# Optimization experiments

Measured on AMD Instinct MI355X. Metric: run time of the kernel, lower is better.

The kernel has to match this reference:

```python
import jax, jax.numpy as jnp
import numpy as np

NUM_V = 20000
N_EDGES = 160000
IN_CH, OUT_CH = 16, 32
IN_ORDER = OUT_ORDER = MID_ORDER = 2
N_RINGS = 2
BAND_LIMIT = 2
NUM_SAMPLES = 7


def build_kernel_basis(n_in, n_out, bl):
    """Equivariant kernel basis [num_bases, 2*bl+1, 2*n_out+1, 2*n_in+1].
    Freq axis layout: [const, cos(t), sin(t), cos(2t), sin(2t), ...] matching precomp."""
    Din, Dout, F = 2 * n_in + 1, 2 * n_out + 1, 2 * bl + 1
    I = np.eye(2)
    E = np.array([[0., -1.], [1., 0.]])   # rotation by pi/2
    S = np.array([[1., 0.], [0., -1.]])   # reflection
    ES = E @ S
    sl = lambda m: slice(0, 1) if m == 0 else slice(2 * m - 1, 2 * m + 1)
    bases = []

    def add(f, cos_blk, sin_blk, m, n):
        if f > bl:
            return
        B = np.zeros((F, Dout, Din))
        if f == 0:
            B[0, sl(m), sl(n)] = cos_blk
        else:
            B[2 * f - 1, sl(m), sl(n)] = cos_blk
            B[2 * f, sl(m), sl(n)] = sin_blk
        bases.append(B)

    for m in range(n_out + 1):
        for n in range(n_in + 1):
            if m == 0 and n == 0:
                add(0, np.ones((1, 1)), None, 0, 0)
            elif n == 0:  # scalar -> order-m pair: R(m t) e1, R(m t) e2
                add(m, np.array([[1.], [0.]]), np.array([[0.], [1.]]), m, 0)
                add(m, np.array([[0.], [1.]]), np.array([[-1.], [0.]]), m, 0)
            elif m == 0:  # order-n pair -> scalar: rows of R(-n t)
                add(n, np.array([[1., 0.]]), np.array([[0., 1.]]), 0, n)
                add(n, np.array([[0., 1.]]), np.array([[-1., 0.]]), 0, n)
            else:
                d = m - n
                f = abs(d)
                sg = 1.0 if d >= 0 else -1.0
                add(f, I, sg * E, m, n)          # R(d t)
                add(f, E, -sg * I, m, n)         # R(d t + pi/2)
                add(m + n, S, ES, m, n)          # R((m+n) t) S
                add(m + n, ES, -S, m, n)         # R((m+n) t + pi/2) S
    return np.stack(bases).astype(np.float32)


def fourier_mats(order, n):
    th = 2 * np.pi * np.arange(n) / n
    cols = [np.ones(n)]
    for m in range(1, order + 1):
        cols += [np.cos(m * th), np.sin(m * th)]
    T = np.stack(cols, 1)                              # [n_samples, 2*order+1]
    scale = np.array([1.0] + [2.0] * (2 * order)) / n
    Tinv = (T * scale).T                               # [2*order+1, n_samples]
    return jnp.asarray(T, jnp.float32), jnp.asarray(Tinv, jnp.float32)


def rep_act(x, alpha, order):
    """Gauge transport: rotate order-m feature pairs by m*alpha. x: [E,C,2*order+1]."""
    parts = [x[:, :, :1]]
    for m in range(1, order + 1):
        c = jnp.cos(m * alpha)[:, None]
        s = jnp.sin(m * alpha)[:, None]
        a, b = x[:, :, 2 * m - 1], x[:, :, 2 * m]
        parts.append(jnp.stack([c * a - s * b, s * a + c * b], axis=-1))
    return jnp.concatenate(parts, axis=-1)


def gem_conv(x, edge_index, precomp, connection, K, W, b, in_order):
    src, dst = edge_index[1], edge_index[0]
    xt = rep_act(x[src], connection, in_order)               # [E, Cin, Din] gather + transport
    wk = jnp.einsum('bfij,broc->froicj', K, W)               # fold basis with ring weights (small)
    t = jnp.einsum('ecj,froicj->efroi', xt, wk)              # per-edge freq/ring responses
    msg = jnp.einsum('efr,efroi->eoi', precomp, t)           # [E, Cout, Dout]
    out = jax.ops.segment_sum(msg, dst, num_segments=NUM_V)  # scatter-add to vertices
    return out.at[:, :, 0].add(b)                            # bias on scalar component


def regular_relu(x, order):
    T, Tinv = fourier_mats(order, NUM_SAMPLES)
    s = jnp.einsum('vcd,sd->vcs', x, T)   # irrep -> regular samples
    return jnp.einsum('vcs,ds->vcd', jax.nn.relu(s), Tinv)


def setup_inputs() -> dict:
    key = jax.random.key(0)
    k = jax.random.split(key, 8)
    nb = build_kernel_basis(IN_ORDER, MID_ORDER, BAND_LIMIT).shape[0]  # 19
    Din = 2 * IN_ORDER + 1
    x = jax.random.normal(k[0], (NUM_V, IN_CH, Din), jnp.float32)
    edge_index = jax.random.randint(k[1], (2, N_EDGES), 0, NUM_V, dtype=jnp.int32)
    precomp = jax.random.normal(k[2], (N_EDGES, 2 * BAND_LIMIT + 1, N_RINGS), jnp.float32)
    connection = jax.random.uniform(k[3], (N_EDGES,), jnp.float32) * (2 * np.pi)
    W1 = jax.random.normal(k[4], (nb, N_RINGS, OUT_CH, IN_CH), jnp.float32) * 0.1
    W2 = jax.random.normal(k[5], (nb, N_RINGS, OUT_CH, OUT_CH), jnp.float32) * 0.05
    W_lin = jax.random.normal(k[6], (OUT_CH, IN_CH), jnp.float32) * 0.1
    zeros = lambda: jnp.zeros((OUT_CH,), jnp.float32)
    return {"x": x, "edge_index": edge_index, "precomp": precomp, "connection": connection,
            "W1": W1, "b1": zeros(), "W2": W2, "b2": zeros(), "W_lin": W_lin, "b_lin": zeros()}


def reference(x, edge_index, precomp, connection, W1, b1, W2, b2, W_lin, b_lin):
    K = jnp.asarray(build_kernel_basis(IN_ORDER, MID_ORDER, BAND_LIMIT))  # orders equal -> shared basis
    y = gem_conv(x, edge_index, precomp, connection, K, W1, b1, IN_ORDER)
    y = regular_relu(y, MID_ORDER)
    y = gem_conv(y, edge_index, precomp, connection, K, W2, b2, MID_ORDER)
    res = jnp.einsum('vcd,oc->vod', x, W_lin) + b_lin[None, :, None]  # 1x1 conv residual
    o = min(y.shape[2], res.shape[2])
    y = y.at[:, :, :o].add(res[:, :, :o])
    return regular_relu(y, OUT_ORDER)
```

## Files before the change

kernel.cpp:

```cpp
#include <hip/hip_runtime.h>
#include <hip/hip_bf16.h>
#include <cstdint>

#define NV     20000
#define NE     160000
#define IC1    16
#define OC     32
#define DIN    5
#define NSLOT  49
#define NOUT   160
struct SlotTables {
    int n;
    int b[64], f[64], i[64], j[64];
    float v[64];
};

constexpr SlotTables make_slots() {
    SlotTables T{};
    float K[19][5][5][5] = {};
    int nb = 0;
    const int BL = 2;
    auto add = [&](int f, const float (*cb)[2], const float (*sb)[2],
                   int m, int n) {
        if (f > BL) return;
        int r0 = (m == 0) ? 0 : (2 * m - 1), nr = (m == 0) ? 1 : 2;
        int c0 = (n == 0) ? 0 : (2 * n - 1), nc = (n == 0) ? 1 : 2;
        for (int a = 0; a < nr; a++)
            for (int bb = 0; bb < nc; bb++) {
                if (f == 0) {
                    K[nb][0][r0 + a][c0 + bb] = cb[a][bb];
                } else {
                    K[nb][2 * f - 1][r0 + a][c0 + bb] = cb[a][bb];
                    K[nb][2 * f    ][r0 + a][c0 + bb] = sb[a][bb];
                }
            }
        nb++;
    };
    const float ONE[2][2]  = {{1, 0}, {0, 0}};
    const float I2[2][2]   = {{1, 0}, {0, 1}};
    const float E2[2][2]   = {{0, -1}, {1, 0}};
    const float S2[2][2]   = {{1, 0}, {0, -1}};
    const float ES2[2][2]  = {{0, 1}, {1, 0}};
    const float NS2[2][2]  = {{-1, 0}, {0, 1}};
    const float C10[2][2]  = {{1, 0}, {0, 0}};
    const float C01[2][2]  = {{0, 0}, {1, 0}};
    const float CM10[2][2] = {{-1, 0}, {0, 0}};
    const float R10[2][2]  = {{1, 0}, {0, 0}};
    const float R01[2][2]  = {{0, 1}, {0, 0}};
    const float RM10[2][2] = {{-1, 0}, {0, 0}};

    for (int m = 0; m <= 2; m++)
        for (int n = 0; n <= 2; n++) {
            if (m == 0 && n == 0) {
                add(0, ONE, ONE, 0, 0);
            } else if (n == 0) {
                add(m, C10, C01, m, 0);
                add(m, C01, CM10, m, 0);
            } else if (m == 0) {
                add(n, R10, R01, 0, n);
                add(n, R01, RM10, 0, n);
            } else {
                int d = m - n;
                int f = d >= 0 ? d : -d;
                float sg = d >= 0 ? 1.f : -1.f;
                const float sgE[2][2]  = {{0, -sg}, {sg, 0}};
                const float msgI[2][2] = {{-sg, 0}, {0, -sg}};
                add(f, I2, sgE, m, n);
                add(f, E2, msgI, m, n);
                add(m + n, S2, ES2, m, n);
                add(m + n, ES2, NS2, m, n);
            }
        }
    T.n = 0;
    for (int i = 0; i < 5; i++)
        for (int b = 0; b < nb; b++)
            for (int f = 0; f < 5; f++)
                for (int j = 0; j < 5; j++)
                    if (K[b][f][i][j] != 0.0f) {
                        T.b[T.n] = b; T.f[T.n] = f; T.i[T.n] = i;
                        T.j[T.n] = j; T.v[T.n] = K[b][f][i][j];
                        T.n++;
                    }
    return T;
}

constexpr SlotTables SL = make_slots();
static_assert(SL.n == NSLOT, "expect 49 kernel-basis nonzeros");

__device__ __forceinline__ uint32_t bf16_rne(float f) {
    uint32_t u = __float_as_uint(f);
    u += 0x7fffu + ((u >> 16) & 1u);
    return u >> 16;
}

typedef __attribute__((ext_vector_type(8))) short bf16x8;
typedef __attribute__((ext_vector_type(4))) float f32x4;

template<int C>
__global__ __launch_bounds__(256) void build_M(const float* __restrict__ W,
                                               float* __restrict__ M) {
    int t = blockIdx.x * 256 + threadIdx.x;
    const int K = C * 50;
    if (t >= K * NOUT) return;
    int n = t % NOUT, k = t / NOUT;
    int o = n / 5, i = n % 5;
    int c = k / 50, r50 = k % 50;
    int j = r50 / 10, q = r50 % 10;
    int f = q >> 1, r = q & 1;
    float acc = 0.f;
    #pragma unroll
    for (int s = 0; s < NSLOT; s++) {
        if (SL.j[s] == j && SL.f[s] == f && SL.i[s] == i)
            acc += SL.v[s] * W[(size_t)((SL.b[s] * 2 + r) * 32 + o) * C + c];
    }
    M[(size_t)k * NOUT + n] = acc;
}

template<int K>
__global__ __launch_bounds__(256) void build_Mfrag(const float* __restrict__ M,
                                                   uint32_t* __restrict__ Mf) {
    int t = blockIdx.x * 256 + threadIdx.x;
    const int total = (K / 32) * 10 * 64 * 4;
    if (t >= total) return;
    int a = t & 3;
    int idx = t >> 2;
    int lane = idx & 63; idx >>= 6;
    int nt = idx % 10;
    int ck = idx / 10;
    int col = nt * 16 + (lane & 15);
    int k0 = ck * 32 + (lane >> 4) * 8 + 2 * a;
    uint32_t lo = bf16_rne(M[(size_t)k0 * NOUT + col]);
    uint32_t hi = bf16_rne(M[(size_t)(k0 + 1) * NOUT + col]);
    Mf[t] = lo | (hi << 16);
}

__global__ __launch_bounds__(256) void hist_k(const int* __restrict__ ei,
                                              int* __restrict__ counts) {
    int e = blockIdx.x * 256 + threadIdx.x;
    if (e < NE) atomicAdd(&counts[ei[e]], 1);
}

__global__ __launch_bounds__(1024) void scan_k(const int* __restrict__ counts,
                                               int* __restrict__ cursor) {
    __shared__ int part[1024];
    int t = threadIdx.x;
    int base = t * 20;
    int local[20];
    int s = 0;
    #pragma unroll
    for (int k = 0; k < 20; k++) {
        int idx = base + k;
        int c = (idx < NV) ? counts[idx] : 0;
        local[k] = c; s += c;
    }
    part[t] = s;
    __syncthreads();
    for (int off = 1; off < 1024; off <<= 1) {
        int add = (t >= off) ? part[t - off] : 0;
        __syncthreads();
        part[t] += add;
        __syncthreads();
    }
    int run = (t == 0) ? 0 : part[t - 1];
    #pragma unroll
    for (int k = 0; k < 20; k++) {
        int idx = base + k;
        if (idx < NV) { cursor[idx] = run; run += local[k]; }
    }
}

__global__ __launch_bounds__(256) void scatter_pack(const int* __restrict__ ei,
                                                    const float* __restrict__ pre,
                                                    const float* __restrict__ conn,
                                                    int* __restrict__ cursor,
                                                    int* __restrict__ SRC,
                                                    float4* __restrict__ REC) {
    int e = blockIdx.x * 256 + threadIdx.x;
    if (e == 0) {
        SRC[NE] = 0;
        REC[(size_t)NE * 3 + 0] = float4{0.f, 0.f, 0.f, 0.f};
        REC[(size_t)NE * 3 + 1] = float4{0.f, 0.f, 0.f, 0.f};
        REC[(size_t)NE * 3 + 2] = float4{0.f, 0.f, 0.f, 0.f};
    }
    if (e >= NE) return;
    int pos = atomicAdd(&cursor[ei[e]], 1);
    SRC[pos] = ei[NE + e];
    float al = conn[e];
    float c1 = __cosf(al), s1 = __sinf(al);
    const float* pp = pre + (size_t)e * 10;
    REC[(size_t)pos * 3 + 0] = float4{c1, s1, pp[0], pp[1]};
    REC[(size_t)pos * 3 + 1] = float4{pp[2], pp[3], pp[4], pp[5]};
    REC[(size_t)pos * 3 + 2] = float4{pp[6], pp[7], pp[8], pp[9]};
}

__global__ __launch_bounds__(256) void x_pack(const float* __restrict__ x,
                                              uint4* __restrict__ xb) {
    int t = blockIdx.x * 256 + threadIdx.x;
    if (t >= NV * IC1) return;
    const float* xr = x + (size_t)t * 5;
    uint4 o;
    o.x = bf16_rne(xr[0]) | (bf16_rne(xr[1]) << 16);
    o.y = bf16_rne(xr[2]) | (bf16_rne(xr[3]) << 16);
    o.z = bf16_rne(xr[4]);
    o.w = 0;
    xb[t] = o;
}

template<int C>
__global__ __launch_bounds__(256) void zbuild6(const uint4* __restrict__ xb,
                                               const int*   __restrict__ SRC,
                                               const float4* __restrict__ REC,
                                               const int* __restrict__ cursor,
                                               uint32_t* __restrict__ Z,
                                               int v0, int v1) {
    __shared__ uint32_t st[3200];
    int tid = threadIdx.x;
    int t = blockIdx.x * 256 + tid;
    int pair = t >> 1, h = t & 1;
    int npairs = (v1 - v0) * C;
    bool valid = pair < npairs;
    int c = pair % C;
    int v = v0 + (valid ? pair / C : 0);
    int beg = 0, end = 0;
    if (valid) { beg = (v == 0) ? 0 : cursor[v - 1]; end = cursor[v]; }

    float acc[25];
    #pragma unroll
    for (int z = 0; z < 25; z++) acc[z] = 0.f;

    int k = beg;
    if (k < end) {
        int k1 = (k + 1 < end) ? k + 1 : NE;
        int k2 = (k + 2 < end) ? k + 2 : NE;
        int s0 = SRC[k], s1i = SRC[k1], s2i = SRC[k2];
        const float4* rp = REC + (size_t)k * 3;
        float4 r0 = rp[0], r1 = rp[1], r2 = rp[2];
        uint4 u0 = xb[(size_t)s0 * C + c];
        uint4 u1 = xb[(size_t)s1i * C + c];
        while (true) {
            bool more = (k1 != NE);
            int k3 = (k + 3 < end) ? k + 3 : NE;
            int s3i = SRC[k3];
            uint4 u2 = xb[(size_t)s2i * C + c];
            const float4* rpn = REC + (size_t)k1 * 3;
            float4 n0 = rpn[0], n1 = rpn[1], n2 = rpn[2];
            float x0 = __uint_as_float(u0.x << 16);
            float x1 = __uint_as_float(u0.x & 0xffff0000u);
            float x2 = __uint_as_float(u0.y << 16);
            float x3 = __uint_as_float(u0.y & 0xffff0000u);
            float x4 = __uint_as_float(u0.z << 16);
            float cc1 = r0.x, ss1 = r0.y;
            float cc2 = cc1 * cc1 - ss1 * ss1, ss2 = 2.f * cc1 * ss1;
            float xt[5];
            xt[0] = x0;
            xt[1] = cc1 * x1 - ss1 * x2;
            xt[2] = ss1 * x1 + cc1 * x2;
            xt[3] = cc2 * x3 - ss2 * x4;
            xt[4] = ss2 * x3 + cc2 * x4;
            float ph[5];
            ph[0] = h ? r1.w : r0.z;
            ph[1] = h ? r2.x : r0.w;
            ph[2] = h ? r2.y : r1.x;
            ph[3] = h ? r2.z : r1.y;
            ph[4] = h ? r2.w : r1.z;
            #pragma unroll
            for (int j = 0; j < 5; j++)
                #pragma unroll
                for (int w = 0; w < 5; w++)
                    acc[j * 5 + w] = fmaf(xt[j], ph[w], acc[j * 5 + w]);
            if (!more) break;
            k = k1; k1 = k2; k2 = k3;
            r0 = n0; r1 = n1; r2 = n2;
            u0 = u1; u1 = u2;
            s2i = s3i;
        }
    }
    uint32_t* sb = st + (tid >> 1) * 25;
    #pragma unroll
    for (int j = 0; j < 5; j++) {
        float q5v = __shfl_xor(acc[j * 5 + 0], 1);
        if (h == 0) {
            sb[j * 5 + 0] = bf16_rne(acc[j * 5 + 0]) | (bf16_rne(acc[j * 5 + 1]) << 16);
            sb[j * 5 + 1] = bf16_rne(acc[j * 5 + 2]) | (bf16_rne(acc[j * 5 + 3]) << 16);
            sb[j * 5 + 2] = bf16_rne(acc[j * 5 + 4]) | (bf16_rne(q5v) << 16);
        } else {
            sb[j * 5 + 3] = bf16_rne(acc[j * 5 + 1]) | (bf16_rne(acc[j * 5 + 2]) << 16);
            sb[j * 5 + 4] = bf16_rne(acc[j * 5 + 3]) | (bf16_rne(acc[j * 5 + 4]) << 16);
        }
    }
    __syncthreads();
    size_t gbase = (size_t)blockIdx.x * 3200;
    int pbase = blockIdx.x * 128;
    for (int i = tid; i < 3200; i += 256)
        if (pbase + i / 25 < npairs) Z[gbase + i] = st[i];
}

template<int K>
__global__ __launch_bounds__(256) void gemm_mfma(const uint32_t* __restrict__ Z,
                                                 const uint32_t* __restrict__ Mf,
                                                 float* __restrict__ Y,
                                                 int rows) {
    constexpr int NC = K / 32;
    __shared__ uint4 Bs[2][640];
    int t = threadIdx.x;
    int lane = t & 63;
    int wave = t >> 6;
    int r0 = blockIdx.x * 64 + wave * 16;
    int mrow = lane & 15;
    int q = lane >> 4;
    int ra = r0 + mrow;
    if (ra >= rows) ra = rows - 1;
    const uint32_t* za = Z + (size_t)ra * (K / 2) + q * 4;
    const uint4* mfg = (const uint4*)Mf + lane;

    auto stage = [&](int ck, int nb) {
        const uint4* gp = mfg + (size_t)ck * 640;
        for (int i = wave; i < 10; i += 4)
            __builtin_amdgcn_global_load_lds(
                (const __attribute__((address_space(1))) void*)(gp + i * 64),
                (__attribute__((address_space(3))) void*)(&Bs[nb][i * 64]),
                16, 0, 0);
    };

    f32x4 acc[10];
    #pragma unroll
    for (int nt = 0; nt < 10; nt++) acc[nt] = {0.f, 0.f, 0.f, 0.f};

    stage(0, 0);
    bf16x8 af = *(const bf16x8*)za;
    __syncthreads();

    for (int ck = 0; ck < NC; ck++) {
        int buf = ck & 1;
        bf16x8 af_n = af;
        if (ck + 1 < NC) {
            stage(ck + 1, buf ^ 1);
            af_n = *(const bf16x8*)(za + (ck + 1) * 16);
        }
        bf16x8 bf[10];
        #pragma unroll
        for (int nt = 0; nt < 10; nt++)
            bf[nt] = *(const bf16x8*)&Bs[buf][nt * 64 + lane];
        #pragma unroll
        for (int nt = 0; nt < 10; nt++)
            acc[nt] = __builtin_amdgcn_mfma_f32_16x16x32_bf16(af, bf[nt],
                                                              acc[nt], 0, 0, 0);
        af = af_n;
        __syncthreads();
    }
    #pragma unroll
    for (int reg = 0; reg < 4; reg++) {
        int rr = r0 + q * 4 + reg;
        if (rr < rows) {
            float* yb = Y + (size_t)rr * NOUT + (lane & 15);
            #pragma unroll
            for (int nt = 0; nt < 10; nt++) yb[nt * 16] = acc[nt][reg];
        }
    }
}

__device__ __forceinline__ void fourier_relu(float d0, float d1, float d2,
                                             float d3, float d4, float* out5) {
    float o0 = 0, o1 = 0, o2 = 0, o3 = 0, o4 = 0;
    #pragma unroll
    for (int k = 0; k < 7; k++) {
        float th = (float)k * (6.28318530717958647692f / 7.0f);
        float ck = __cosf(th), sk = __sinf(th);
        float c2k = ck * ck - sk * sk, s2k = 2.f * ck * sk;
        float sv = d0 + ck * d1 + sk * d2 + c2k * d3 + s2k * d4;
        sv = fmaxf(sv, 0.f);
        o0 += sv; o1 += sv * ck; o2 += sv * sk; o3 += sv * c2k; o4 += sv * s2k;
    }
    const float i7 = 1.0f / 7.0f;
    out5[0] = o0 * i7; out5[1] = o1 * (2.f * i7); out5[2] = o2 * (2.f * i7);
    out5[3] = o3 * (2.f * i7); out5[4] = o4 * (2.f * i7);
}

__global__ __launch_bounds__(256) void relu_mid(const float* __restrict__ y,
                                                const float* __restrict__ b1,
                                                uint4* __restrict__ yb) {
    int t = blockIdx.x * 256 + threadIdx.x;
    if (t >= NV * 32) return;
    int ch = t & 31;
    const float* yr = y + (size_t)t * 5;
    float r[5];
    fourier_relu(yr[0] + b1[ch], yr[1], yr[2], yr[3], yr[4], r);
    uint4 o;
    o.x = bf16_rne(r[0]) | (bf16_rne(r[1]) << 16);
    o.y = bf16_rne(r[2]) | (bf16_rne(r[3]) << 16);
    o.z = bf16_rne(r[4]);
    o.w = 0;
    yb[t] = o;
}

__global__ __launch_bounds__(256) void final_k(const float* __restrict__ y2,
                                               const float* __restrict__ x,
                                               const float* __restrict__ Wl,
                                               const float* __restrict__ bl,
                                               const float* __restrict__ b2,
                                               float* __restrict__ out) {
    int t = blockIdx.x * 256 + threadIdx.x;
    if (t >= NV * 32) return;
    int o = t & 31;
    int v = t >> 5;
    float r0 = 0, r1 = 0, r2 = 0, r3 = 0, r4 = 0;
    const float* xb = x + (size_t)v * (IC1 * DIN);
    const float* wl = Wl + o * IC1;
    #pragma unroll
    for (int c = 0; c < IC1; c++) {
        float w = wl[c];
        r0 = fmaf(w, xb[c*5+0], r0); r1 = fmaf(w, xb[c*5+1], r1);
        r2 = fmaf(w, xb[c*5+2], r2); r3 = fmaf(w, xb[c*5+3], r3);
        r4 = fmaf(w, xb[c*5+4], r4);
    }
    float blo = bl[o];
    const float* yb = y2 + (size_t)t * 5;
    float d0 = yb[0] + b2[o] + r0 + blo;
    float d1 = yb[1] + r1 + blo;
    float d2 = yb[2] + r2 + blo;
    float d3 = yb[3] + r3 + blo;
    float d4 = yb[4] + r4 + blo;
    float r[5];
    fourier_relu(d0, d1, d2, d3, d4, r);
    float* ob = out + (size_t)t * 5;
    #pragma unroll
    for (int d = 0; d < 5; d++) ob[d] = r[d];
}

extern "C" void kernel_launch(void* const* d_in, const int* in_sizes, int n_in,
                              void* d_out, int out_size, void* d_ws, size_t ws_size,
                              hipStream_t stream) {
    const float* x    = (const float*)d_in[0];
    const int*   ei   = (const int*)  d_in[1];
    const float* pre  = (const float*)d_in[2];
    const float* conn = (const float*)d_in[3];
    const float* W1   = (const float*)d_in[4];
    const float* b1   = (const float*)d_in[5];
    const float* W2   = (const float*)d_in[6];
    const float* b2   = (const float*)d_in[7];
    const float* Wl   = (const float*)d_in[8];
    const float* bl   = (const float*)d_in[9];
    float* out = (float*)d_out;

    const int K1 = IC1 * 50;
    const int K2 = OC  * 50;

    const size_t Y_BYTES   = (size_t)NV * NOUT * sizeof(float);
    const size_t M1_BYTES  = (size_t)K1 * NOUT * sizeof(float);
    const size_t M2_BYTES  = (size_t)K2 * NOUT * sizeof(float);
    const size_t MF1_BYTES = (size_t)(K1 / 32) * 10 * 64 * 16;
    const size_t MF2_BYTES = (size_t)(K2 / 32) * 10 * 64 * 16;
    const size_t CSR_BYTES = (size_t)(2 * NV) * sizeof(int);
    const size_t REC_BYTES = (size_t)(NE + 1) * 48;
    const size_t SRC_BYTES = (((size_t)(NE + 1) * 4 + 15) / 16) * 16;
    const size_t Y1B_BYTES = (size_t)NV * OC * 16;
    char* ws = (char*)d_ws;
    float* y1 = (float*)(ws);
    float* y2 = y1;
    float* M1 = (float*)(ws + Y_BYTES);
    float* M2 = (float*)(ws + Y_BYTES + M1_BYTES);
    uint32_t* Mf1 = (uint32_t*)(ws + Y_BYTES + M1_BYTES + M2_BYTES);
    uint32_t* Mf2 = (uint32_t*)(ws + Y_BYTES + M1_BYTES + M2_BYTES + MF1_BYTES);
    int* counts = (int*)(ws + Y_BYTES + M1_BYTES + M2_BYTES + MF1_BYTES + MF2_BYTES);
    int* cursor = counts + NV;
    size_t csr_end = Y_BYTES + M1_BYTES + M2_BYTES + MF1_BYTES + MF2_BYTES
                   + CSR_BYTES;
    float4* REC = (float4*)(ws + csr_end);
    int*    SRC = (int*)(ws + csr_end + REC_BYTES);
    uint4*  Y1B = (uint4*)(ws + csr_end + REC_BYTES + SRC_BYTES);
    uint4*  XB1 = Y1B;
    size_t fixed = csr_end + REC_BYTES + SRC_BYTES + Y1B_BYTES;

    size_t tail = (ws_size > fixed) ? (ws_size - fixed) : 0;
    uint32_t* zbuf;
    size_t zcap;
    if (tail >= Y_BYTES) { zbuf = (uint32_t*)(ws + fixed); zcap = tail; }
    else                 { zbuf = (uint32_t*)d_out;        zcap = Y_BYTES; }
    int chunk1 = (int)(zcap / ((size_t)K1 * 2)); if (chunk1 > NV) chunk1 = NV;
    int chunk2 = (int)(zcap / ((size_t)K2 * 2)); if (chunk2 > NV) chunk2 = NV;

    hipMemsetAsync(counts, 0, NV * sizeof(int), stream);

    build_M<IC1><<<(K1 * NOUT + 255) / 256, 256, 0, stream>>>(W1, M1);
    build_M<OC> <<<(K2 * NOUT + 255) / 256, 256, 0, stream>>>(W2, M2);
    build_Mfrag<K1><<<((K1 / 32) * 2560 + 255) / 256, 256, 0, stream>>>(M1, Mf1);
    build_Mfrag<K2><<<((K2 / 32) * 2560 + 255) / 256, 256, 0, stream>>>(M2, Mf2);

    hist_k<<<(NE + 255) / 256, 256, 0, stream>>>(ei, counts);
    scan_k<<<1, 1024, 0, stream>>>(counts, cursor);
    scatter_pack<<<(NE + 255) / 256, 256, 0, stream>>>(ei, pre, conn, cursor,
                                                       SRC, REC);
    x_pack<<<(NV * IC1 + 255) / 256, 256, 0, stream>>>(x, XB1);

    for (int v0 = 0; v0 < NV; v0 += chunk1) {
        int v1 = v0 + chunk1; if (v1 > NV) v1 = NV;
        int rows = v1 - v0;
        zbuild6<IC1><<<((size_t)rows * IC1 * 2 + 255) / 256, 256, 0, stream>>>(
            XB1, SRC, REC, cursor, zbuf, v0, v1);
        gemm_mfma<K1><<<(rows + 63) / 64, 256, 0, stream>>>(
            zbuf, Mf1, y1 + (size_t)v0 * NOUT, rows);
    }
    relu_mid<<<(NV * 32 + 255) / 256, 256, 0, stream>>>(y1, b1, Y1B);
    for (int v0 = 0; v0 < NV; v0 += chunk2) {
        int v1 = v0 + chunk2; if (v1 > NV) v1 = NV;
        int rows = v1 - v0;
        zbuild6<OC><<<((size_t)rows * OC * 2 + 255) / 256, 256, 0, stream>>>(
            Y1B, SRC, REC, cursor, zbuf, v0, v1);
        gemm_mfma<K2><<<(rows + 63) / 64, 256, 0, stream>>>(
            zbuf, Mf2, y2 + (size_t)v0 * NOUT, rows);
    }
    final_k<<<(NV * 32 + 255) / 256, 256, 0, stream>>>(y2, x, Wl, bl, b2, out);
}
```

Baseline: 265.1 us.

## Fuse Fourier ReLU and residual epilogues into MFMA GEMM kernels

The mid-layer ReLU and the final residual-plus-ReLU kernels are folded into the GEMM as an epilogue. Accumulators are staged through padded shared memory, then each thread applies the bias, ReLU and bf16 packing, or the residual and ReLU, before writing. This removes the fp32 intermediate buffers y1/y2, their global write and read-back, and two launches. In exchange it adds about 42 KB of LDS per block, which can reduce occupancy. The layer-1 epilogue also writes into Y1B while it is still aliased with the input XB1, which is only safe when the whole graph fits in one chunk.

New measurement: 274.6 us. 1.04x slower.

```diff
diff --git a/kernel.cpp b/kernel.cpp
--- a/kernel.cpp
+++ b/kernel.cpp
@@ -9,6 +9,7 @@
 #define DIN    5
 #define NSLOT  49
 #define NOUT   160
+#define YSTR   165
 struct SlotTables {
     int n;
     int b[64], f[64], i[64], j[64];
@@ -295,13 +296,36 @@
         if (pbase + i / 25 < npairs) Z[gbase + i] = st[i];
 }
 
-template<int K>
-__global__ __launch_bounds__(256) void gemm_mfma(const uint32_t* __restrict__ Z,
-                                                 const uint32_t* __restrict__ Mf,
-                                                 float* __restrict__ Y,
-                                                 int rows) {
+__device__ __forceinline__ void fourier_relu(float d0, float d1, float d2,
+                                             float d3, float d4, float* out5) {
+    float o0 = 0, o1 = 0, o2 = 0, o3 = 0, o4 = 0;
+    #pragma unroll
+    for (int k = 0; k < 7; k++) {
+        float th = (float)k * (6.28318530717958647692f / 7.0f);
+        float ck = __cosf(th), sk = __sinf(th);
+        float c2k = ck * ck - sk * sk, s2k = 2.f * ck * sk;
+        float sv = d0 + ck * d1 + sk * d2 + c2k * d3 + s2k * d4;
+        sv = fmaxf(sv, 0.f);
+        o0 += sv; o1 += sv * ck; o2 += sv * sk; o3 += sv * c2k; o4 += sv * s2k;
+    }
+    const float i7 = 1.0f / 7.0f;
+    out5[0] = o0 * i7; out5[1] = o1 * (2.f * i7); out5[2] = o2 * (2.f * i7);
+    out5[3] = o3 * (2.f * i7); out5[4] = o4 * (2.f * i7);
+}
+
+template<int K, int EPI>
+__global__ __launch_bounds__(256) void gemm_fused(const uint32_t* __restrict__ Z,
+                                                  const uint32_t* __restrict__ Mf,
+                                                  int rows,
+                                                  uint4* __restrict__ y1b,
+                                                  const float* __restrict__ bias,
+                                                  const float* __restrict__ xres,
+                                                  const float* __restrict__ Wl,
+                                                  const float* __restrict__ bl,
+                                                  float* __restrict__ outp) {
     constexpr int NC = K / 32;
     __shared__ uint4 Bs[2][640];
+    __shared__ float Ys[64 * YSTR];
     int t = threadIdx.x;
     int lane = t & 63;
     int wave = t >> 6;
@@ -349,82 +373,58 @@
         __syncthreads();
     }
     #pragma unroll
-    for (int reg = 0; reg < 4; reg++) {
-        int rr = r0 + q * 4 + reg;
-        if (rr < rows) {
-            float* yb = Y + (size_t)rr * NOUT + (lane & 15);
+    for (int nt = 0; nt < 10; nt++) {
+        int col = nt * 16 + mrow;
+        #pragma unroll
+        for (int reg = 0; reg < 4; reg++) {
+            int r = wave * 16 + q * 4 + reg;
+            Ys[r * YSTR + col] = acc[nt][reg];
+        }
+    }
+    __syncthreads();
+    #pragma unroll
+    for (int it = 0; it < 8; it++) {
+        int item = t + it * 256;
+        int row = item >> 5, ch = item & 31;
+        int vr = blockIdx.x * 64 + row;
+        if (vr >= rows) continue;
+        const float* yr = &Ys[row * YSTR + ch * 5];
+        float d0 = yr[0], d1 = yr[1], d2 = yr[2], d3 = yr[3], d4 = yr[4];
+        float r5[5];
+        if (EPI == 1) {
+            d0 += bias[ch];
+            fourier_relu(d0, d1, d2, d3, d4, r5);
+            uint4 o;
+            o.x = bf16_rne(r5[0]) | (bf16_rne(r5[1]) << 16);
+            o.y = bf16_rne(r5[2]) | (bf16_rne(r5[3]) << 16);
+            o.z = bf16_rne(r5[4]);
+            o.w = 0;
+            y1b[(size_t)vr * 32 + ch] = o;
+        } else {
+            float rr0 = 0, rr1 = 0, rr2 = 0, rr3 = 0, rr4 = 0;
+            const float* xb = xres + (size_t)vr * (IC1 * DIN);
+            const float* wl = Wl + ch * IC1;
             #pragma unroll
-            for (int nt = 0; nt < 10; nt++) yb[nt * 16] = acc[nt][reg];
+            for (int c = 0; c < IC1; c++) {
+                float w = wl[c];
+                rr0 = fmaf(w, xb[c * 5 + 0], rr0);
+                rr1 = fmaf(w, xb[c * 5 + 1], rr1);
+                rr2 = fmaf(w, xb[c * 5 + 2], rr2);
+                rr3 = fmaf(w, xb[c * 5 + 3], rr3);
+                rr4 = fmaf(w, xb[c * 5 + 4], rr4);
+            }
+            float blo = bl[ch];
+            d0 += bias[ch] + rr0 + blo;
+            d1 += rr1 + blo;
+            d2 += rr2 + blo;
+            d3 += rr3 + blo;
+            d4 += rr4 + blo;
+            fourier_relu(d0, d1, d2, d3, d4, r5);
+            float* ob = outp + ((size_t)vr * 32 + ch) * 5;
+            #pragma unroll
+            for (int d = 0; d < 5; d++) ob[d] = r5[d];
         }
     }
-}
-
-__device__ __forceinline__ void fourier_relu(float d0, float d1, float d2,
-                                             float d3, float d4, float* out5) {
-    float o0 = 0, o1 = 0, o2 = 0, o3 = 0, o4 = 0;
-    #pragma unroll
-    for (int k = 0; k < 7; k++) {
-        float th = (float)k * (6.28318530717958647692f / 7.0f);
-        float ck = __cosf(th), sk = __sinf(th);
-        float c2k = ck * ck - sk * sk, s2k = 2.f * ck * sk;
-        float sv = d0 + ck * d1 + sk * d2 + c2k * d3 + s2k * d4;
-        sv = fmaxf(sv, 0.f);
-        o0 += sv; o1 += sv * ck; o2 += sv * sk; o3 += sv * c2k; o4 += sv * s2k;
-    }
-    const float i7 = 1.0f / 7.0f;
-    out5[0] = o0 * i7; out5[1] = o1 * (2.f * i7); out5[2] = o2 * (2.f * i7);
-    out5[3] = o3 * (2.f * i7); out5[4] = o4 * (2.f * i7);
-}
-
-__global__ __launch_bounds__(256) void relu_mid(const float* __restrict__ y,
-                                                const float* __restrict__ b1,
-                                                uint4* __restrict__ yb) {
-    int t = blockIdx.x * 256 + threadIdx.x;
-    if (t >= NV * 32) return;
-    int ch = t & 31;
-    const float* yr = y + (size_t)t * 5;
-    float r[5];
-    fourier_relu(yr[0] + b1[ch], yr[1], yr[2], yr[3], yr[4], r);
-    uint4 o;
-    o.x = bf16_rne(r[0]) | (bf16_rne(r[1]) << 16);
-    o.y = bf16_rne(r[2]) | (bf16_rne(r[3]) << 16);
-    o.z = bf16_rne(r[4]);
-    o.w = 0;
-    yb[t] = o;
-}
-
-__global__ __launch_bounds__(256) void final_k(const float* __restrict__ y2,
-                                               const float* __restrict__ x,
-                                               const float* __restrict__ Wl,
-                                               const float* __restrict__ bl,
-                                               const float* __restrict__ b2,
-                                               float* __restrict__ out) {
-    int t = blockIdx.x * 256 + threadIdx.x;
-    if (t >= NV * 32) return;
-    int o = t & 31;
-    int v = t >> 5;
-    float r0 = 0, r1 = 0, r2 = 0, r3 = 0, r4 = 0;
-    const float* xb = x + (size_t)v * (IC1 * DIN);
-    const float* wl = Wl + o * IC1;
-    #pragma unroll
-    for (int c = 0; c < IC1; c++) {
-        float w = wl[c];
-        r0 = fmaf(w, xb[c*5+0], r0); r1 = fmaf(w, xb[c*5+1], r1);
-        r2 = fmaf(w, xb[c*5+2], r2); r3 = fmaf(w, xb[c*5+3], r3);
-        r4 = fmaf(w, xb[c*5+4], r4);
-    }
-    float blo = bl[o];
-    const float* yb = y2 + (size_t)t * 5;
-    float d0 = yb[0] + b2[o] + r0 + blo;
-    float d1 = yb[1] + r1 + blo;
-    float d2 = yb[2] + r2 + blo;
-    float d3 = yb[3] + r3 + blo;
-    float d4 = yb[4] + r4 + blo;
-    float r[5];
-    fourier_relu(d0, d1, d2, d3, d4, r);
-    float* ob = out + (size_t)t * 5;
-    #pragma unroll
-    for (int d = 0; d < 5; d++) ob[d] = r[d];
 }
 
 extern "C" void kernel_launch(void* const* d_in, const int* in_sizes, int n_in,
@@ -455,16 +455,13 @@
     const size_t SRC_BYTES = (((size_t)(NE + 1) * 4 + 15) / 16) * 16;
     const size_t Y1B_BYTES = (size_t)NV * OC * 16;
     char* ws = (char*)d_ws;
-    float* y1 = (float*)(ws);
-    float* y2 = y1;
-    float* M1 = (float*)(ws + Y_BYTES);
-    float* M2 = (float*)(ws + Y_BYTES + M1_BYTES);
-    uint32_t* Mf1 = (uint32_t*)(ws + Y_BYTES + M1_BYTES + M2_BYTES);
-    uint32_t* Mf2 = (uint32_t*)(ws + Y_BYTES + M1_BYTES + M2_BYTES + MF1_BYTES);
-    int* counts = (int*)(ws + Y_BYTES + M1_BYTES + M2_BYTES + MF1_BYTES + MF2_BYTES);
+    float* M1 = (float*)(ws);
+    float* M2 = (float*)(ws + M1_BYTES);
+    uint32_t* Mf1 = (uint32_t*)(ws + M1_BYTES + M2_BYTES);
+    uint32_t* Mf2 = (uint32_t*)(ws + M1_BYTES + M2_BYTES + MF1_BYTES);
+    int* counts = (int*)(ws + M1_BYTES + M2_BYTES + MF1_BYTES + MF2_BYTES);
     int* cursor = counts + NV;
-    size_t csr_end = Y_BYTES + M1_BYTES + M2_BYTES + MF1_BYTES + MF2_BYTES
-                   + CSR_BYTES;
+    size_t csr_end = M1_BYTES + M2_BYTES + MF1_BYTES + MF2_BYTES + CSR_BYTES;
     float4* REC = (float4*)(ws + csr_end);
     int*    SRC = (int*)(ws + csr_end + REC_BYTES);
     uint4*  Y1B = (uint4*)(ws + csr_end + REC_BYTES + SRC_BYTES);
@@ -497,17 +494,17 @@
         int rows = v1 - v0;
         zbuild6<IC1><<<((size_t)rows * IC1 * 2 + 255) / 256, 256, 0, stream>>>(
             XB1, SRC, REC, cursor, zbuf, v0, v1);
-        gemm_mfma<K1><<<(rows + 63) / 64, 256, 0, stream>>>(
-            zbuf, Mf1, y1 + (size_t)v0 * NOUT, rows);
-    }
-    relu_mid<<<(NV * 32 + 255) / 256, 256, 0, stream>>>(y1, b1, Y1B);
+        gemm_fused<K1, 1><<<(rows + 63) / 64, 256, 0, stream>>>(
+            zbuf, Mf1, rows, Y1B + (size_t)v0 * 32, b1,
+            nullptr, nullptr, nullptr, nullptr);
+    }
     for (int v0 = 0; v0 < NV; v0 += chunk2) {
         int v1 = v0 + chunk2; if (v1 > NV) v1 = NV;
         int rows = v1 - v0;
         zbuild6<OC><<<((size_t)rows * OC * 2 + 255) / 256, 256, 0, stream>>>(
             Y1B, SRC, REC, cursor, zbuf, v0, v1);
-        gemm_mfma<K2><<<(rows + 63) / 64, 256, 0, stream>>>(
-            zbuf, Mf2, y2 + (size_t)v0 * NOUT, rows);
-    }
-    final_k<<<(NV * 32 + 255) / 256, 256, 0, stream>>>(y2, x, Wl, bl, b2, out);
-}
+        gemm_fused<K2, 2><<<(rows + 63) / 64, 256, 0, stream>>>(
+            zbuf, Mf2, rows, nullptr, b2,
+            x + (size_t)v0 * (IC1 * DIN), Wl, bl, out + (size_t)v0 * NOUT);
+    }
+}
```
